# Performance work log

Hardware: AMD Instinct MI355X
Metric: run time of the kernel (lower is better)

Reference implementation:

```python
import jax, jax.numpy as jnp
import numpy as np

ALPHA = 1.5
BETA = 45.0
LAMDA = 0.5
B = 8192   # batch_size
D = 128    # feature dim (hardcoded in original via zeros((1,128)))
V = 4      # number of views stacked in fj
EPS = 1e-12  # F.normalize eps


def _l2norm_rows(x):
    n = jnp.sqrt(jnp.sum(x * x, axis=-1, keepdims=True))
    return x / jnp.maximum(n, EPS)


def setup_inputs() -> dict:
    key = jax.random.key(0)
    k1, k2 = jax.random.split(key)
    fi = jax.random.normal(k1, (B, D), dtype=jnp.float32)
    fj = jax.random.normal(k2, (V, B, D), dtype=jnp.float32)
    # L2-normalize embeddings so exp(beta*(SVM - lamda)) stays finite (beta=45)
    fi = _l2norm_rows(fi)
    fj = _l2norm_rows(fj)
    return {"fi": fi, "fj": fj, "b": V}


def avg_svm(fi, fj):
    # Original: per-row softmax-weighted average of fj rows, renormalized,
    # dotted with fi row, averaged over the batch.
    A = fi @ fj.T                      # [B, B] pairwise logits
    W = jax.nn.softmax(A, axis=1)      # softmax over j (alphalist / sumofalpha)
    Vw = W @ fj                        # [B, D] softmax-weighted averages
    Vn = _l2norm_rows(Vw)              # F.normalize(p=2, dim=1)
    return jnp.mean(jnp.sum(fi * Vn, axis=1))  # mean_i fi[i] . Vn[i]


def reference(fi, fj, b):
    b = int(b)
    # SMM1 is recomputed identically every outer iteration in the original;
    # compute once and multiply the per-iteration term by (b-1).
    smm1 = avg_svm(fi, fi)
    if b > 2:
        # inner loop: SMM2sum is a running (cumulative) sum over j=1..b-2,
        # and exp(beta*(SMM2sum - lamda)) is added at every step.
        s_vals = jnp.stack([avg_svm(fi, fj[j]) for j in range(1, b - 1)])
        cum = jnp.cumsum(s_vals)
        ssum = jnp.sum(jnp.exp(BETA * (cum - LAMDA)))
    else:
        ssum = jnp.exp(BETA * (avg_svm(fi, fj) - LAMDA))
    term = (1.0 / ALPHA) * jnp.log1p(jnp.exp(-ALPHA * (smm1 - LAMDA))) \
         + (1.0 / BETA) * jnp.log1p(ssum)
    loss = (b - 1) * term
    return jnp.squeeze(loss)
```

## Files before the change

kernel.cpp:

```cpp
#include <hip/hip_runtime.h>

#define BDIM 8192
#define DDIM 128

typedef __attribute__((ext_vector_type(4))) float floatx4;
typedef long i64;

#define SLAB (BDIM * DDIM)
#define G8_OFF 64
#define G8T_OFF (64 + 3 * SLAB)

__device__ inline void load_lds16(const void* g, void* l) {
    __builtin_amdgcn_global_load_lds(
        (const __attribute__((address_space(1))) unsigned int*)g,
        (__attribute__((address_space(3))) unsigned int*)l, 16, 0, 0);
}

__global__ __launch_bounds__(256)
void prep_kernel(const float* __restrict__ fi, const float* __restrict__ fj,
                 unsigned char* __restrict__ g8, unsigned char* __restrict__ g8T,
                 float* __restrict__ acc)
{
    const int p = blockIdx.y;
    const int kblock = blockIdx.x;
    const int rbase = kblock * 32;
    const int tid = threadIdx.x;
    if (p == 0 && kblock == 0 && tid < 8) acc[tid] = 0.f;
    const float* src = (p == 0) ? fi : (fj + (size_t)p * SLAB);

    __shared__ __align__(16) unsigned char T8[32][144];

    {
        const int row = tid >> 3, c = tid & 7;
        const float* sp = src + (size_t)(rbase + row) * DDIM + c * 16;
        float4 f0 = ((const float4*)sp)[0];
        float4 f1 = ((const float4*)sp)[1];
        float4 f2 = ((const float4*)sp)[2];
        float4 f3 = ((const float4*)sp)[3];
        alignas(16) int w[4];
        w[0] = __builtin_amdgcn_cvt_pk_fp8_f32(f0.x, f0.y, 0, false);
        w[0] = __builtin_amdgcn_cvt_pk_fp8_f32(f0.z, f0.w, w[0], true);
        w[1] = __builtin_amdgcn_cvt_pk_fp8_f32(f1.x, f1.y, 0, false);
        w[1] = __builtin_amdgcn_cvt_pk_fp8_f32(f1.z, f1.w, w[1], true);
        w[2] = __builtin_amdgcn_cvt_pk_fp8_f32(f2.x, f2.y, 0, false);
        w[2] = __builtin_amdgcn_cvt_pk_fp8_f32(f2.z, f2.w, w[2], true);
        w[3] = __builtin_amdgcn_cvt_pk_fp8_f32(f3.x, f3.y, 0, false);
        w[3] = __builtin_amdgcn_cvt_pk_fp8_f32(f3.z, f3.w, w[3], true);
        int4 v = *(int4*)w;
        *(int4*)(g8 + (size_t)p * SLAB + (size_t)(rbase + row) * DDIM + c * 16) = v;
        *(int4*)(&T8[row][c * 16]) = v;
    }
    __syncthreads();
    {
        const int d = tid >> 1, half = tid & 1;
        alignas(16) unsigned char bb[16];
        #pragma unroll
        for (int i = 0; i < 16; ++i) bb[i] = T8[half * 16 + i][d];
        *(int4*)(g8T + (size_t)p * SLAB + (size_t)kblock * 4096 + d * 32 + half * 16) =
            *(int4*)bb;
    }
}

__global__ __launch_bounds__(256, 3)
void flash_kernel(const float* __restrict__ fi,
                  const unsigned char* __restrict__ g8,
                  const unsigned char* __restrict__ g8T,
                  float* __restrict__ acc)
{
    const int b = blockIdx.x;
    const int gp = (b & 7) * 96 + (b >> 3);
    const int p = gp >> 8;
    const int qbase = (gp & 255) * 32;
    const int tid = threadIdx.x;
    const int wave = tid >> 6, lane = tid & 63;
    const int quad = lane >> 4, col = lane & 15;

    __shared__ __align__(16) char smem[38400];
    #define KOFF 0
    #define VOFF 16384
    #define POFF 32768
    #define DOFF 37120
    #define NOFF 37760

    const unsigned char* g8p  = g8  + (size_t)p * SLAB;
    const unsigned char* g8Tp = g8T + (size_t)p * SLAB;

    i64 qf[2][4];
    #pragma unroll
    for (int qt = 0; qt < 2; ++qt)
        #pragma unroll
        for (int kk = 0; kk < 4; ++kk)
            qf[qt][kk] = *(const i64*)(g8 + (size_t)(qbase + qt * 16 + col) * DDIM +
                                       kk * 32 + quad * 8);

    floatx4 O[2][2];
    #pragma unroll
    for (int qt = 0; qt < 2; ++qt)
        #pragma unroll
        for (int j = 0; j < 2; ++j)
            O[qt][j] = (floatx4){0.f, 0.f, 0.f, 0.f};

    auto stageK = [&](int kb) {
        #pragma unroll
        for (int i = 0; i < 4; ++i) {
            int s = i * 64 + lane;
            int key = s >> 3, cp = s & 7;
            int c = cp ^ (key & 7);
            const unsigned char* gp8 = g8p +
                (size_t)(kb + wave * 32 + key) * DDIM + c * 16;
            load_lds16(gp8, smem + KOFF + wave * 4096 + i * 1024);
        }
    };
    auto stageV = [&](int kb) {
        #pragma unroll
        for (int i = 0; i < 4; ++i) {
            int s = wave * 256 + i * 64 + lane;
            int d = s >> 3, cp = s & 7;
            int c = cp ^ (d & 7);
            const unsigned char* gp8 = g8Tp +
                (size_t)((kb >> 5) + (c >> 1)) * 4096 + d * 32 + (c & 1) * 16;
            load_lds16(gp8, smem + VOFF + wave * 4096 + i * 1024);
        }
    };

    stageK(0);
    stageV(0);
    __syncthreads();

    for (int k = 0; k < 64; ++k) {
        floatx4 S[2][2];
        #pragma unroll
        for (int kt = 0; kt < 2; ++kt)
            #pragma unroll
            for (int qt = 0; qt < 2; ++qt)
                S[kt][qt] = (floatx4){0.f, 0.f, 0.f, 0.f};
        #pragma unroll
        for (int kk = 0; kk < 4; ++kk) {
            i64 kf[2];
            #pragma unroll
            for (int kt = 0; kt < 2; ++kt) {
                int key = kt * 16 + col;
                int cU = (kk * 2 + (quad >> 1)) ^ (key & 7);
                kf[kt] = *(const i64*)(smem + KOFF + wave * 4096 +
                                       (key * 8 + cU) * 16 + (quad & 1) * 8);
            }
            #pragma unroll
            for (int qt = 0; qt < 2; ++qt) {
                S[0][qt] = __builtin_amdgcn_mfma_f32_16x16x32_fp8_fp8(
                    kf[0], qf[qt][kk], S[0][qt], 0, 0, 0);
                S[1][qt] = __builtin_amdgcn_mfma_f32_16x16x32_fp8_fp8(
                    kf[1], qf[qt][kk], S[1][qt], 0, 0, 0);
            }
        }

        if (k + 1 < 64) stageK((k + 1) * 128);

        #pragma unroll
        for (int kt = 0; kt < 2; ++kt)
            #pragma unroll
            for (int qt = 0; qt < 2; ++qt) {
                int v = __builtin_amdgcn_cvt_pk_fp8_f32(
                    __expf(fminf(S[kt][qt][0], 4.f)),
                    __expf(fminf(S[kt][qt][1], 4.f)), 0, false);
                v = __builtin_amdgcn_cvt_pk_fp8_f32(
                    __expf(fminf(S[kt][qt][2], 4.f)),
                    __expf(fminf(S[kt][qt][3], 4.f)), v, true);
                *(int*)(smem + POFF + (qt * 16 + col) * 136 +
                        wave * 32 + kt * 16 + quad * 4) = v;
            }

        __syncthreads();

        #pragma unroll
        for (int kc = 0; kc < 4; ++kc) {
            i64 pf[2];
            #pragma unroll
            for (int qt = 0; qt < 2; ++qt)
                pf[qt] = *(const i64*)(smem + POFF + (qt * 16 + col) * 136 +
                                       kc * 32 + quad * 8);
            i64 vf[2];
            #pragma unroll
            for (int j = 0; j < 2; ++j) {
                int d = (wave * 2 + j) * 16 + col;
                int c = (kc * 2 + (quad >> 1)) ^ (d & 7);
                vf[j] = *(const i64*)(smem + VOFF + (d * 8 + c) * 16 +
                                      (quad & 1) * 8);
            }
            #pragma unroll
            for (int qt = 0; qt < 2; ++qt)
                #pragma unroll
                for (int j = 0; j < 2; ++j)
                    O[qt][j] = __builtin_amdgcn_mfma_f32_16x16x32_fp8_fp8(
                        pf[qt], vf[j], O[qt][j], 0, 0, 0);
        }

        __syncthreads();

        if (k + 1 < 64) stageV((k + 1) * 128);
    }

    float* pdot = (float*)(smem + DOFF);
    float* pnrm = (float*)(smem + NOFF);
    #pragma unroll
    for (int qt = 0; qt < 2; ++qt)
        #pragma unroll
        for (int r = 0; r < 4; ++r) {
            const int q = qt * 16 + quad * 4 + r;
            float dot = 0.f, nr = 0.f;
            #pragma unroll
            for (int j = 0; j < 2; ++j) {
                float o = O[qt][j][r];
                float fq = fi[(size_t)(qbase + q) * DDIM + (wave * 2 + j) * 16 + col];
                dot += fq * o;
                nr += o * o;
            }
            #pragma unroll
            for (int m = 1; m < 16; m <<= 1) {
                dot += __shfl_xor(dot, m, 64);
                nr  += __shfl_xor(nr,  m, 64);
            }
            if (col == 0) {
                pdot[wave * 32 + q] = dot;
                pnrm[wave * 32 + q] = nr;
            }
        }
    __syncthreads();
    if (tid < 32) {
        const int q = tid;
        float D = pdot[q] + pdot[32 + q] + pdot[64 + q] + pdot[96 + q];
        float N = pnrm[q] + pnrm[32 + q] + pnrm[64 + q] + pnrm[96 + q];
        float val = D * rsqrtf(fmaxf(N, 1e-30f));
        #pragma unroll
        for (int m = 1; m < 32; m <<= 1) val += __shfl_xor(val, m, 64);
        if (tid == 0) atomicAdd(&acc[p], val);
    }
}

__global__ void final_kernel(const float* __restrict__ acc, float* __restrict__ out)
{
    if (threadIdx.x == 0 && blockIdx.x == 0) {
        const double s0 = (double)acc[0] / (double)BDIM;
        const double s1 = (double)acc[1] / (double)BDIM;
        const double s2 = (double)acc[2] / (double)BDIM;
        const double t1 = (1.0 / 1.5) * log1p(exp(-1.5 * (s0 - 0.5)));
        const double ssum = exp(45.0 * (s1 - 0.5)) + exp(45.0 * (s1 + s2 - 0.5));
        const double t2 = (1.0 / 45.0) * log1p(ssum);
        out[0] = (float)(3.0 * (t1 + t2));
    }
}

extern "C" void kernel_launch(void* const* d_in, const int* in_sizes, int n_in,
                              void* d_out, int out_size, void* d_ws, size_t ws_size,
                              hipStream_t stream)
{
    const float* fi = (const float*)d_in[0];
    const float* fj = (const float*)d_in[1];

    float* acc = (float*)d_ws;
    unsigned char* g8  = (unsigned char*)d_ws + G8_OFF;
    unsigned char* g8T = (unsigned char*)d_ws + G8T_OFF;

    prep_kernel <<<dim3(BDIM / 32, 3), 256, 0, stream>>>(fi, fj, g8, g8T, acc);
    flash_kernel<<<dim3(768), 256, 0, stream>>>(fi, g8, g8T, acc);
    final_kernel<<<1, 64, 0, stream>>>(acc, (float*)d_out);
}
```

Measured before the change: 172.1 us.

## Switch fp8 MFMAs to 16x16x128 scaled f8f6f4 instructions with swizzled P tile

Replaces the four 16x16x32 fp8 MFMAs per K-chunk with a single 16x16x128 scaled f8f6f4 MFMA (unit scales), loading 32-byte operand pairs from LDS as two 16-byte reads. The P staging buffer drops its row padding in favor of an XOR swizzle so the wider reads avoid bank conflicts, shrinking LDS slightly. This aims to cut MFMA issue count and LDS instruction count on gfx950, at the risk of the k-ordering of paired chunks not matching between operands.

```diff
diff --git a/kernel.cpp b/kernel.cpp
--- a/kernel.cpp
+++ b/kernel.cpp
@@ -4,7 +4,8 @@
 #define DDIM 128
 
 typedef __attribute__((ext_vector_type(4))) float floatx4;
-typedef long i64;
+typedef __attribute__((ext_vector_type(4))) int   intx4;
+typedef __attribute__((ext_vector_type(8))) int   intx8;
 
 #define SLAB (BDIM * DDIM)
 #define G8_OFF 64
@@ -14,6 +15,13 @@
     __builtin_amdgcn_global_load_lds(
         (const __attribute__((address_space(1))) unsigned int*)g,
         (__attribute__((address_space(3))) unsigned int*)l, 16, 0, 0);
+}
+
+__device__ inline intx8 ld_pair(const char* base, int c0) {
+    union { intx8 v; intx4 h[2]; } u;
+    u.h[0] = *(const intx4*)(base + c0 * 16);
+    u.h[1] = *(const intx4*)(base + (c0 ^ 1) * 16);
+    return u.v;
 }
 
 __global__ __launch_bounds__(256)
@@ -75,23 +83,26 @@
     const int wave = tid >> 6, lane = tid & 63;
     const int quad = lane >> 4, col = lane & 15;
 
-    __shared__ __align__(16) char smem[38400];
+    __shared__ __align__(16) char smem[37888];
     #define KOFF 0
     #define VOFF 16384
     #define POFF 32768
-    #define DOFF 37120
-    #define NOFF 37760
+    #define DOFF 36864
+    #define NOFF 37376
 
     const unsigned char* g8p  = g8  + (size_t)p * SLAB;
     const unsigned char* g8Tp = g8T + (size_t)p * SLAB;
 
-    i64 qf[2][4];
+    intx8 qf[2];
     #pragma unroll
-    for (int qt = 0; qt < 2; ++qt)
-        #pragma unroll
-        for (int kk = 0; kk < 4; ++kk)
-            qf[qt][kk] = *(const i64*)(g8 + (size_t)(qbase + qt * 16 + col) * DDIM +
-                                       kk * 32 + quad * 8);
+    for (int qt = 0; qt < 2; ++qt) {
+        const intx4* qp = (const intx4*)(g8 + (size_t)(qbase + qt * 16 + col) * DDIM +
+                                         quad * 32);
+        union { intx8 v; intx4 h[2]; } u;
+        u.h[0] = qp[0];
+        u.h[1] = qp[1];
+        qf[qt] = u.v;
+    }
 
     floatx4 O[2][2];
     #pragma unroll
@@ -130,27 +141,17 @@
     for (int k = 0; k < 64; ++k) {
         floatx4 S[2][2];
         #pragma unroll
-        for (int kt = 0; kt < 2; ++kt)
+        for (int kt = 0; kt < 2; ++kt) {
+            const int key = kt * 16 + col;
+            const int c0 = (quad * 2) ^ (key & 7);
+            intx8 kf = ld_pair(smem + KOFF + wave * 4096 + key * 128, c0);
             #pragma unroll
             for (int qt = 0; qt < 2; ++qt)
-                S[kt][qt] = (floatx4){0.f, 0.f, 0.f, 0.f};
-        #pragma unroll
-        for (int kk = 0; kk < 4; ++kk) {
-            i64 kf[2];
-            #pragma unroll
-            for (int kt = 0; kt < 2; ++kt) {
-                int key = kt * 16 + col;
-                int cU = (kk * 2 + (quad >> 1)) ^ (key & 7);
-                kf[kt] = *(const i64*)(smem + KOFF + wave * 4096 +
-                                       (key * 8 + cU) * 16 + (quad & 1) * 8);
-            }
-            #pragma unroll
-            for (int qt = 0; qt < 2; ++qt) {
-                S[0][qt] = __builtin_amdgcn_mfma_f32_16x16x32_fp8_fp8(
-                    kf[0], qf[qt][kk], S[0][qt], 0, 0, 0);
-                S[1][qt] = __builtin_amdgcn_mfma_f32_16x16x32_fp8_fp8(
-                    kf[1], qf[qt][kk], S[1][qt], 0, 0, 0);
-            }
+                S[kt][qt] = __builtin_amdgcn_mfma_scale_f32_16x16x128_f8f6f4(
+                    kf, qf[qt], (floatx4){0.f, 0.f, 0.f, 0.f},
+                    0, 0,
+                    0, 127,
+                    0, 127);
         }
 
         if (k + 1 < 64) stageK((k + 1) * 128);
@@ -165,33 +166,29 @@
                 v = __builtin_amdgcn_cvt_pk_fp8_f32(
                     __expf(fminf(S[kt][qt][2], 4.f)),
                     __expf(fminf(S[kt][qt][3], 4.f)), v, true);
-                *(int*)(smem + POFF + (qt * 16 + col) * 136 +
-                        wave * 32 + kt * 16 + quad * 4) = v;
+                const int q = qt * 16 + col;
+                *(int*)(smem + POFF + q * 128 +
+                        (((wave * 2 + kt) ^ (q & 7)) * 16) + quad * 4) = v;
             }
 
         __syncthreads();
 
-        #pragma unroll
-        for (int kc = 0; kc < 4; ++kc) {
-            i64 pf[2];
-            #pragma unroll
-            for (int qt = 0; qt < 2; ++qt)
-                pf[qt] = *(const i64*)(smem + POFF + (qt * 16 + col) * 136 +
-                                       kc * 32 + quad * 8);
-            i64 vf[2];
+        {
+            intx8 vf[2];
             #pragma unroll
             for (int j = 0; j < 2; ++j) {
-                int d = (wave * 2 + j) * 16 + col;
-                int c = (kc * 2 + (quad >> 1)) ^ (d & 7);
-                vf[j] = *(const i64*)(smem + VOFF + (d * 8 + c) * 16 +
-                                      (quad & 1) * 8);
-            }
-            #pragma unroll
-            for (int qt = 0; qt < 2; ++qt)
+                const int d = (wave * 2 + j) * 16 + col;
+                vf[j] = ld_pair(smem + VOFF + d * 128, (quad * 2) ^ (d & 7));
+            }
+            #pragma unroll
+            for (int qt = 0; qt < 2; ++qt) {
+                const int q = qt * 16 + col;
+                intx8 pf = ld_pair(smem + POFF + q * 128, (quad * 2) ^ (q & 7));
                 #pragma unroll
                 for (int j = 0; j < 2; ++j)
-                    O[qt][j] = __builtin_amdgcn_mfma_f32_16x16x32_fp8_fp8(
-                        pf[qt], vf[j], O[qt][j], 0, 0, 0);
+                    O[qt][j] = __builtin_amdgcn_mfma_scale_f32_16x16x128_f8f6f4(
+                        pf, vf[j], O[qt][j], 0, 0, 0, 127, 0, 127);
+            }
         }
 
         __syncthreads();
```

After: 158.1 us. 8.2% less time.
